# Performance work log

Measured on AMD Instinct MI355X. Metric: run time of the kernel, lower is better.

Reference implementation:

```python
import jax, jax.numpy as jnp
import numpy as np

S, D_MODEL, D_K = 4096, 1024, 64
SCALE = float(np.sqrt(D_K))


def setup_inputs() -> dict:
    key = jax.random.key(0)
    ks = jax.random.split(key, 7)
    def p(k, shape, fan_in):
        # torch nn.Linear default init: U(-1/sqrt(fan_in), 1/sqrt(fan_in))
        lim = 1.0 / np.sqrt(fan_in)
        return jax.random.uniform(k, shape, jnp.float32, -lim, lim)
    return {
        "x": jax.random.normal(ks[0], (S, D_MODEL), jnp.float32),
        "Wq": p(ks[1], (D_K, D_MODEL), D_MODEL),
        "bq": p(ks[2], (D_K,), D_MODEL),
        "Wk": p(ks[3], (D_K, D_MODEL), D_MODEL),
        "bk": p(ks[4], (D_K,), D_MODEL),
        "Wv": p(ks[5], (D_K, D_MODEL), D_MODEL),
        "bv": p(ks[6], (D_K,), D_MODEL),
    }


def reference(x, Wq, bq, Wk, bk, Wv, bv):
    # Linear projections: y = x @ W.T + b  (torch nn.Linear convention)
    Q = x @ Wq.T + bq          # [S, d_k]
    K = x @ Wk.T + bk          # [S, d_k]
    V = x @ Wv.T + bv          # [S, d_k]
    scores = (Q @ K.T) / SCALE  # [S, S]
    # causal mask: -inf strictly above the diagonal (triu(1))
    row = jnp.arange(S)[:, None]
    col = jnp.arange(S)[None, :]
    scores = jnp.where(col > row, -jnp.inf, scores)
    attn = jax.nn.softmax(scores, axis=1)
    return attn @ V            # [S, d_k]
```

## Files before the change

### kernel.cpp

```cpp
#include <hip/hip_runtime.h>

#define SS 4096
#define DM 1024

typedef __attribute__((ext_vector_type(4))) float f32x4;
typedef __attribute__((ext_vector_type(8))) __bf16 bf16x8;
typedef __attribute__((ext_vector_type(8))) unsigned short ushort8;
typedef __attribute__((ext_vector_type(4))) unsigned short ushort4v;

#define NEGHUGE -3.0e38f
#define LOG2E 1.44269504f

__device__ __forceinline__ unsigned short f2b(float f) {
    unsigned u = __builtin_bit_cast(unsigned, f);
    u += 0x7fffu + ((u >> 16) & 1u);
    return (unsigned short)(u >> 16);
}

__device__ __forceinline__ f32x4 mfma16(ushort8 a, ushort8 b, f32x4 c) {
    return __builtin_amdgcn_mfma_f32_16x16x32_bf16(
        __builtin_bit_cast(bf16x8, a), __builtin_bit_cast(bf16x8, b), c, 0, 0, 0);
}

__global__ __launch_bounds__(256) void convw_kernel(
    const float* __restrict__ Wq, const float* __restrict__ Wk,
    const float* __restrict__ Wv, unsigned short* __restrict__ wb)
{
    int i = (blockIdx.x * 256 + threadIdx.x) * 4;
    const float* src;
    if (i < 65536) src = Wq + i;
    else if (i < 131072) src = Wk + (i - 65536);
    else src = Wv + (i - 131072);
    f32x4 v = *reinterpret_cast<const f32x4*>(src);
    ushort4v o;
    o[0] = f2b(v[0]); o[1] = f2b(v[1]); o[2] = f2b(v[2]); o[3] = f2b(v[3]);
    *reinterpret_cast<ushort4v*>(wb + i) = o;
}

__global__ __launch_bounds__(512) void proj_kernel(
    const float* __restrict__ x, const unsigned short* __restrict__ wb,
    const float* __restrict__ bq, const float* __restrict__ bk, const float* __restrict__ bv,
    unsigned short* __restrict__ Qs, unsigned short* __restrict__ Kb,
    unsigned short* __restrict__ VT)
{
    __shared__ float comb[8 * 3072];
    const int m0 = blockIdx.x * 16;
    const int tid = threadIdx.x;
    const int w = tid >> 6, l = tid & 63;
    const int lc = l & 15;
    const int lk = (l >> 4) * 8;

    f32x4 acc[12] = {};
    const float* xrow = x + (m0 + lc) * DM;
    const int kbase = w * 128;

    for (int kk = 0; kk < 128; kk += 32) {
        const int k0 = kbase + kk + lk;
        f32x4 u = *reinterpret_cast<const f32x4*>(xrow + k0);
        f32x4 v = *reinterpret_cast<const f32x4*>(xrow + k0 + 4);
        ushort8 a;
        a[0] = f2b(u[0]); a[1] = f2b(u[1]); a[2] = f2b(u[2]); a[3] = f2b(u[3]);
        a[4] = f2b(v[0]); a[5] = f2b(v[1]); a[6] = f2b(v[2]); a[7] = f2b(v[3]);
#pragma unroll
        for (int nf = 0; nf < 12; nf++) {
            ushort8 b = *reinterpret_cast<const ushort8*>(wb + (nf * 16 + lc) * DM + k0);
            acc[nf] = mfma16(a, b, acc[nf]);
        }
    }

#pragma unroll
    for (int nf = 0; nf < 12; nf++)
#pragma unroll
        for (int r = 0; r < 4; r++) {
            int row = (l >> 4) * 4 + r;
            comb[w * 3072 + row * 192 + nf * 16 + lc] = acc[nf][r];
        }
    __syncthreads();

    for (int idx = tid; idx < 3072; idx += 512) {
        int row = idx / 192, col = idx % 192;
        float s = 0.f;
#pragma unroll
        for (int ww = 0; ww < 8; ww++) s += comb[ww * 3072 + idx];
        int grow = m0 + row;
        if (col < 64) {
            s += bq[col];
            Qs[grow * 64 + col] = f2b(s * 0.125f);
        } else if (col < 128) {
            s += bk[col - 64];
            Kb[grow * 64 + col - 64] = f2b(s);
        } else {
            s += bv[col - 128];
            VT[(col - 128) * SS + grow] = f2b(s);
        }
    }
}

__global__ __launch_bounds__(256) void attn_part_kernel(
    const unsigned short* __restrict__ Qs, const unsigned short* __restrict__ Kb,
    const unsigned short* __restrict__ VT, float* __restrict__ part)
{
    __shared__ unsigned short plds[4][16 * 64];
    __shared__ float comb[4][16 * 66];

    const int bid = blockIdx.x;
    const int g = bid >> 2, c = bid & 3;
    const int q0 = g * 16;
    const int tid = threadIdx.x;
    const int w = tid >> 6, l = tid & 63;
    const int lc = l & 15;
    const int lg4 = l >> 4;
    const int lk = lg4 * 8;

    const int T = g / 4 + 1;
    const int W0 = c * 4 + w;

    ushort8 aq0 = *reinterpret_cast<const ushort8*>(Qs + (q0 + lc) * 64 + lk);
    ushort8 aq1 = *reinterpret_cast<const ushort8*>(Qs + (q0 + lc) * 64 + 32 + lk);

    float m4[4], l4[4];
    f32x4 o[4] = {};
#pragma unroll
    for (int r = 0; r < 4; r++) { m4[r] = NEGHUGE; l4[r] = 0.f; }

    char* myp = reinterpret_cast<char*>(plds[w]);

    for (int t = W0; t < T; t += 16) {
        const int kv0 = t * 64;
        f32x4 s[4] = {};
#pragma unroll
        for (int nf = 0; nf < 4; nf++) {
            const unsigned short* kr = Kb + (kv0 + nf * 16 + lc) * 64;
            ushort8 b0 = *reinterpret_cast<const ushort8*>(kr + lk);
            ushort8 b1 = *reinterpret_cast<const ushort8*>(kr + 32 + lk);
            s[nf] = mfma16(aq0, b0, s[nf]);
            s[nf] = mfma16(aq1, b1, s[nf]);
        }
        if (kv0 + 63 > q0) {
#pragma unroll
            for (int nf = 0; nf < 4; nf++)
#pragma unroll
                for (int r = 0; r < 4; r++) {
                    int colg = kv0 + nf * 16 + lc;
                    int rowg = q0 + lg4 * 4 + r;
                    if (colg > rowg) s[nf][r] = NEGHUGE;
                }
        }
#pragma unroll
        for (int r = 0; r < 4; r++) {
            float mx = fmaxf(fmaxf(s[0][r], s[1][r]), fmaxf(s[2][r], s[3][r]));
            mx = fmaxf(mx, __shfl_xor(mx, 1));
            mx = fmaxf(mx, __shfl_xor(mx, 2));
            mx = fmaxf(mx, __shfl_xor(mx, 4));
            mx = fmaxf(mx, __shfl_xor(mx, 8));
            float mn = fmaxf(m4[r], mx);
            float sc = exp2f((m4[r] - mn) * LOG2E);
            m4[r] = mn;
            float rs = 0.f;
#pragma unroll
            for (int nf = 0; nf < 4; nf++) {
                float p = exp2f((s[nf][r] - mn) * LOG2E);
                s[nf][r] = p;
                rs += p;
            }
            rs += __shfl_xor(rs, 1);
            rs += __shfl_xor(rs, 2);
            rs += __shfl_xor(rs, 4);
            rs += __shfl_xor(rs, 8);
            l4[r] = l4[r] * sc + rs;
            o[0][r] *= sc; o[1][r] *= sc; o[2][r] *= sc; o[3][r] *= sc;
        }
#pragma unroll
        for (int nf = 0; nf < 4; nf++)
#pragma unroll
            for (int r = 0; r < 4; r++) {
                int row = lg4 * 4 + r;
                int byte = (row * 128 + (nf * 16 + lc) * 2) ^ ((row & 7) << 4);
                *reinterpret_cast<unsigned short*>(myp + byte) = f2b(s[nf][r]);
            }
        asm volatile("s_waitcnt lgkmcnt(0)" ::: "memory");
        __builtin_amdgcn_sched_barrier(0);
#pragma unroll
        for (int k = 0; k < 2; k++) {
            int rbyte = (lc * 128 + (k * 32 + lk) * 2) ^ ((lc & 7) << 4);
            ushort8 pa = *reinterpret_cast<const ushort8*>(myp + rbyte);
#pragma unroll
            for (int df = 0; df < 4; df++) {
                ushort8 bv = *reinterpret_cast<const ushort8*>(
                    VT + (df * 16 + lc) * SS + kv0 + k * 32 + lk);
                o[df] = mfma16(pa, bv, o[df]);
            }
        }
    }

#pragma unroll
    for (int df = 0; df < 4; df++)
#pragma unroll
        for (int r = 0; r < 4; r++)
            comb[w][(lg4 * 4 + r) * 66 + df * 16 + lc] = o[df][r];
    if (lc == 0) {
#pragma unroll
        for (int r = 0; r < 4; r++) {
            comb[w][(lg4 * 4 + r) * 66 + 64] = m4[r];
            comb[w][(lg4 * 4 + r) * 66 + 65] = l4[r];
        }
    }
    __syncthreads();

    float* pp = part + bid * 1056;
    for (int idx = tid; idx < 1024; idx += 256) {
        int row = idx >> 6, col = idx & 63;
        float M = fmaxf(fmaxf(comb[0][row * 66 + 64], comb[1][row * 66 + 64]),
                        fmaxf(comb[2][row * 66 + 64], comb[3][row * 66 + 64]));
        float val = 0.f, den = 0.f;
#pragma unroll
        for (int ww = 0; ww < 4; ww++) {
            float f = exp2f((comb[ww][row * 66 + 64] - M) * LOG2E);
            val += comb[ww][row * 66 + col] * f;
            den += comb[ww][row * 66 + 65] * f;
        }
        pp[row * 66 + col] = val;
        if (col == 0) {
            pp[row * 66 + 64] = M;
            pp[row * 66 + 65] = den;
        }
    }
}

__global__ __launch_bounds__(256) void attn_comb_kernel(
    const float* __restrict__ part, float* __restrict__ out)
{
    const int g = blockIdx.x;
    const int q0 = g * 16;
    const float* p0 = part + (g * 4) * 1056;
    for (int idx = threadIdx.x; idx < 1024; idx += 256) {
        int row = idx >> 6, col = idx & 63;
        float M = NEGHUGE;
#pragma unroll
        for (int cc = 0; cc < 4; cc++)
            M = fmaxf(M, p0[cc * 1056 + row * 66 + 64]);
        float val = 0.f, den = 0.f;
#pragma unroll
        for (int cc = 0; cc < 4; cc++) {
            float f = exp2f((p0[cc * 1056 + row * 66 + 64] - M) * LOG2E);
            val += p0[cc * 1056 + row * 66 + col] * f;
            den += p0[cc * 1056 + row * 66 + 65] * f;
        }
        out[(q0 + row) * 64 + col] = val / den;
    }
}

extern "C" void kernel_launch(void* const* d_in, const int* in_sizes, int n_in,
                              void* d_out, int out_size, void* d_ws, size_t ws_size,
                              hipStream_t stream) {
    const float* x  = (const float*)d_in[0];
    const float* Wq = (const float*)d_in[1];
    const float* bq = (const float*)d_in[2];
    const float* Wk = (const float*)d_in[3];
    const float* bk = (const float*)d_in[4];
    const float* Wv = (const float*)d_in[5];
    const float* bv = (const float*)d_in[6];
    float* out = (float*)d_out;

    char* ws = (char*)d_ws;
    unsigned short* wb = (unsigned short*)ws;
    unsigned short* Qs = (unsigned short*)(ws + 393216);
    unsigned short* Kb = (unsigned short*)(ws + 917504);
    unsigned short* VT = (unsigned short*)(ws + 1441792);
    float* part = (float*)(ws + 1966080);

    convw_kernel<<<dim3(192), dim3(256), 0, stream>>>(Wq, Wk, Wv, wb);
    proj_kernel<<<dim3(256), dim3(512), 0, stream>>>(x, wb, bq, bk, bv, Qs, Kb, VT);
    attn_part_kernel<<<dim3(1024), dim3(256), 0, stream>>>(Qs, Kb, VT, part);
    attn_comb_kernel<<<dim3(256), dim3(256), 0, stream>>>(part, out);
}
```

Baseline: 56.03 us.

## Process 32 query rows per attention block, split KV eight ways, reverse block order

The attention partial kernel now handles 32 query rows per block as two 16-row MFMA tiles that share each K and V fragment load, which halves K/V global traffic per query row. The KV range is split across 8 blocks of 4 waves, and blocks are ordered so the heaviest causal rows launch first. The combine kernel is adjusted to match. The projection kernel is also cut to 4 waves, each doing twice the K-depth, with a padded LDS reduction buffer. The trade-offs are higher register pressure from doubled accumulators and more partial results to merge.

```diff
diff --git a/kernel.cpp b/kernel.cpp
--- a/kernel.cpp
+++ b/kernel.cpp
@@ -2,6 +2,9 @@
 
 #define SS 4096
 #define DM 1024
+#define QBLK 32
+#define CH 8
+#define PSTRIDE 2112
 
 typedef __attribute__((ext_vector_type(4))) float f32x4;
 typedef __attribute__((ext_vector_type(8))) __bf16 bf16x8;
@@ -37,13 +40,13 @@
     *reinterpret_cast<ushort4v*>(wb + i) = o;
 }
 
-__global__ __launch_bounds__(512) void proj_kernel(
+__global__ __launch_bounds__(256) void proj_kernel(
     const float* __restrict__ x, const unsigned short* __restrict__ wb,
     const float* __restrict__ bq, const float* __restrict__ bk, const float* __restrict__ bv,
     unsigned short* __restrict__ Qs, unsigned short* __restrict__ Kb,
     unsigned short* __restrict__ VT)
 {
-    __shared__ float comb[8 * 3072];
+    __shared__ float comb[4 * 16 * 196];
     const int m0 = blockIdx.x * 16;
     const int tid = threadIdx.x;
     const int w = tid >> 6, l = tid & 63;
@@ -52,9 +55,9 @@
 
     f32x4 acc[12] = {};
     const float* xrow = x + (m0 + lc) * DM;
-    const int kbase = w * 128;
-
-    for (int kk = 0; kk < 128; kk += 32) {
+    const int kbase = w * 256;
+
+    for (int kk = 0; kk < 256; kk += 32) {
         const int k0 = kbase + kk + lk;
         f32x4 u = *reinterpret_cast<const f32x4*>(xrow + k0);
         f32x4 v = *reinterpret_cast<const f32x4*>(xrow + k0 + 4);
@@ -73,15 +76,14 @@
 #pragma unroll
         for (int r = 0; r < 4; r++) {
             int row = (l >> 4) * 4 + r;
-            comb[w * 3072 + row * 192 + nf * 16 + lc] = acc[nf][r];
+            comb[w * 3136 + row * 196 + nf * 16 + lc] = acc[nf][r];
         }
     __syncthreads();
 
-    for (int idx = tid; idx < 3072; idx += 512) {
+    for (int idx = tid; idx < 3072; idx += 256) {
         int row = idx / 192, col = idx % 192;
-        float s = 0.f;
-#pragma unroll
-        for (int ww = 0; ww < 8; ww++) s += comb[ww * 3072 + idx];
+        int off = row * 196 + col;
+        float s = comb[off] + comb[3136 + off] + comb[6272 + off] + comb[9408 + off];
         int grow = m0 + row;
         if (col < 64) {
             s += bq[col];
@@ -100,115 +102,141 @@
     const unsigned short* __restrict__ Qs, const unsigned short* __restrict__ Kb,
     const unsigned short* __restrict__ VT, float* __restrict__ part)
 {
-    __shared__ unsigned short plds[4][16 * 64];
-    __shared__ float comb[4][16 * 66];
+    __shared__ unsigned short plds[4][QBLK * 64];
+    __shared__ float comb[4][QBLK * 66];
 
     const int bid = blockIdx.x;
-    const int g = bid >> 2, c = bid & 3;
-    const int q0 = g * 16;
+    const int g = 127 - (bid >> 3);
+    const int c = bid & 7;
+    const int q0 = g * QBLK;
     const int tid = threadIdx.x;
     const int w = tid >> 6, l = tid & 63;
     const int lc = l & 15;
     const int lg4 = l >> 4;
     const int lk = lg4 * 8;
 
-    const int T = g / 4 + 1;
+    const int T = (g + 2) >> 1;
     const int W0 = c * 4 + w;
 
-    ushort8 aq0 = *reinterpret_cast<const ushort8*>(Qs + (q0 + lc) * 64 + lk);
-    ushort8 aq1 = *reinterpret_cast<const ushort8*>(Qs + (q0 + lc) * 64 + 32 + lk);
-
-    float m4[4], l4[4];
-    f32x4 o[4] = {};
-#pragma unroll
-    for (int r = 0; r < 4; r++) { m4[r] = NEGHUGE; l4[r] = 0.f; }
+    ushort8 aq[2][2];
+#pragma unroll
+    for (int rs = 0; rs < 2; rs++) {
+        aq[rs][0] = *reinterpret_cast<const ushort8*>(Qs + (q0 + rs * 16 + lc) * 64 + lk);
+        aq[rs][1] = *reinterpret_cast<const ushort8*>(Qs + (q0 + rs * 16 + lc) * 64 + 32 + lk);
+    }
+
+    float m4[2][4], l4[2][4];
+    f32x4 o[2][4] = {};
+#pragma unroll
+    for (int rs = 0; rs < 2; rs++)
+#pragma unroll
+        for (int r = 0; r < 4; r++) { m4[rs][r] = NEGHUGE; l4[rs][r] = 0.f; }
 
     char* myp = reinterpret_cast<char*>(plds[w]);
 
-    for (int t = W0; t < T; t += 16) {
+    for (int t = W0; t < T; t += 32) {
         const int kv0 = t * 64;
-        f32x4 s[4] = {};
+        f32x4 s[2][4] = {};
 #pragma unroll
         for (int nf = 0; nf < 4; nf++) {
             const unsigned short* kr = Kb + (kv0 + nf * 16 + lc) * 64;
             ushort8 b0 = *reinterpret_cast<const ushort8*>(kr + lk);
             ushort8 b1 = *reinterpret_cast<const ushort8*>(kr + 32 + lk);
-            s[nf] = mfma16(aq0, b0, s[nf]);
-            s[nf] = mfma16(aq1, b1, s[nf]);
+            s[0][nf] = mfma16(aq[0][0], b0, s[0][nf]);
+            s[0][nf] = mfma16(aq[0][1], b1, s[0][nf]);
+            s[1][nf] = mfma16(aq[1][0], b0, s[1][nf]);
+            s[1][nf] = mfma16(aq[1][1], b1, s[1][nf]);
         }
         if (kv0 + 63 > q0) {
 #pragma unroll
+            for (int rs = 0; rs < 2; rs++)
+#pragma unroll
+                for (int nf = 0; nf < 4; nf++)
+#pragma unroll
+                    for (int r = 0; r < 4; r++) {
+                        int colg = kv0 + nf * 16 + lc;
+                        int rowg = q0 + rs * 16 + lg4 * 4 + r;
+                        if (colg > rowg) s[rs][nf][r] = NEGHUGE;
+                    }
+        }
+#pragma unroll
+        for (int rs = 0; rs < 2; rs++)
+#pragma unroll
+            for (int r = 0; r < 4; r++) {
+                float mx = fmaxf(fmaxf(s[rs][0][r], s[rs][1][r]),
+                                 fmaxf(s[rs][2][r], s[rs][3][r]));
+                mx = fmaxf(mx, __shfl_xor(mx, 1));
+                mx = fmaxf(mx, __shfl_xor(mx, 2));
+                mx = fmaxf(mx, __shfl_xor(mx, 4));
+                mx = fmaxf(mx, __shfl_xor(mx, 8));
+                float mn = fmaxf(m4[rs][r], mx);
+                float sc = exp2f((m4[rs][r] - mn) * LOG2E);
+                m4[rs][r] = mn;
+                float rsum = 0.f;
+#pragma unroll
+                for (int nf = 0; nf < 4; nf++) {
+                    float p = exp2f((s[rs][nf][r] - mn) * LOG2E);
+                    s[rs][nf][r] = p;
+                    rsum += p;
+                }
+                rsum += __shfl_xor(rsum, 1);
+                rsum += __shfl_xor(rsum, 2);
+                rsum += __shfl_xor(rsum, 4);
+                rsum += __shfl_xor(rsum, 8);
+                l4[rs][r] = l4[rs][r] * sc + rsum;
+                o[rs][0][r] *= sc; o[rs][1][r] *= sc;
+                o[rs][2][r] *= sc; o[rs][3][r] *= sc;
+            }
+#pragma unroll
+        for (int rs = 0; rs < 2; rs++)
+#pragma unroll
             for (int nf = 0; nf < 4; nf++)
 #pragma unroll
                 for (int r = 0; r < 4; r++) {
-                    int colg = kv0 + nf * 16 + lc;
-                    int rowg = q0 + lg4 * 4 + r;
-                    if (colg > rowg) s[nf][r] = NEGHUGE;
+                    int row = rs * 16 + lg4 * 4 + r;
+                    int byte = (row * 128 + (nf * 16 + lc) * 2) ^ ((row & 7) << 4);
+                    *reinterpret_cast<unsigned short*>(myp + byte) = f2b(s[rs][nf][r]);
                 }
-        }
-#pragma unroll
-        for (int r = 0; r < 4; r++) {
-            float mx = fmaxf(fmaxf(s[0][r], s[1][r]), fmaxf(s[2][r], s[3][r]));
-            mx = fmaxf(mx, __shfl_xor(mx, 1));
-            mx = fmaxf(mx, __shfl_xor(mx, 2));
-            mx = fmaxf(mx, __shfl_xor(mx, 4));
-            mx = fmaxf(mx, __shfl_xor(mx, 8));
-            float mn = fmaxf(m4[r], mx);
-            float sc = exp2f((m4[r] - mn) * LOG2E);
-            m4[r] = mn;
-            float rs = 0.f;
-#pragma unroll
-            for (int nf = 0; nf < 4; nf++) {
-                float p = exp2f((s[nf][r] - mn) * LOG2E);
-                s[nf][r] = p;
-                rs += p;
-            }
-            rs += __shfl_xor(rs, 1);
-            rs += __shfl_xor(rs, 2);
-            rs += __shfl_xor(rs, 4);
-            rs += __shfl_xor(rs, 8);
-            l4[r] = l4[r] * sc + rs;
-            o[0][r] *= sc; o[1][r] *= sc; o[2][r] *= sc; o[3][r] *= sc;
-        }
-#pragma unroll
-        for (int nf = 0; nf < 4; nf++)
-#pragma unroll
-            for (int r = 0; r < 4; r++) {
-                int row = lg4 * 4 + r;
-                int byte = (row * 128 + (nf * 16 + lc) * 2) ^ ((row & 7) << 4);
-                *reinterpret_cast<unsigned short*>(myp + byte) = f2b(s[nf][r]);
-            }
         asm volatile("s_waitcnt lgkmcnt(0)" ::: "memory");
         __builtin_amdgcn_sched_barrier(0);
 #pragma unroll
         for (int k = 0; k < 2; k++) {
-            int rbyte = (lc * 128 + (k * 32 + lk) * 2) ^ ((lc & 7) << 4);
-            ushort8 pa = *reinterpret_cast<const ushort8*>(myp + rbyte);
+            ushort8 pa0, pa1;
+            {
+                int rb0 = ((lc) * 128 + (k * 32 + lk) * 2) ^ ((lc & 7) << 4);
+                int rb1 = ((16 + lc) * 128 + (k * 32 + lk) * 2) ^ ((lc & 7) << 4);
+                pa0 = *reinterpret_cast<const ushort8*>(myp + rb0);
+                pa1 = *reinterpret_cast<const ushort8*>(myp + rb1);
+            }
 #pragma unroll
             for (int df = 0; df < 4; df++) {
                 ushort8 bv = *reinterpret_cast<const ushort8*>(
                     VT + (df * 16 + lc) * SS + kv0 + k * 32 + lk);
-                o[df] = mfma16(pa, bv, o[df]);
+                o[0][df] = mfma16(pa0, bv, o[0][df]);
+                o[1][df] = mfma16(pa1, bv, o[1][df]);
             }
         }
     }
 
 #pragma unroll
-    for (int df = 0; df < 4; df++)
-#pragma unroll
-        for (int r = 0; r < 4; r++)
-            comb[w][(lg4 * 4 + r) * 66 + df * 16 + lc] = o[df][r];
-    if (lc == 0) {
-#pragma unroll
-        for (int r = 0; r < 4; r++) {
-            comb[w][(lg4 * 4 + r) * 66 + 64] = m4[r];
-            comb[w][(lg4 * 4 + r) * 66 + 65] = l4[r];
+    for (int rs = 0; rs < 2; rs++) {
+#pragma unroll
+        for (int df = 0; df < 4; df++)
+#pragma unroll
+            for (int r = 0; r < 4; r++)
+                comb[w][(rs * 16 + lg4 * 4 + r) * 66 + df * 16 + lc] = o[rs][df][r];
+        if (lc == 0) {
+#pragma unroll
+            for (int r = 0; r < 4; r++) {
+                comb[w][(rs * 16 + lg4 * 4 + r) * 66 + 64] = m4[rs][r];
+                comb[w][(rs * 16 + lg4 * 4 + r) * 66 + 65] = l4[rs][r];
+            }
         }
     }
     __syncthreads();
 
-    float* pp = part + bid * 1056;
-    for (int idx = tid; idx < 1024; idx += 256) {
+    float* pp = part + bid * PSTRIDE;
+    for (int idx = tid; idx < QBLK * 64; idx += 256) {
         int row = idx >> 6, col = idx & 63;
         float M = fmaxf(fmaxf(comb[0][row * 66 + 64], comb[1][row * 66 + 64]),
                         fmaxf(comb[2][row * 66 + 64], comb[3][row * 66 + 64]));
@@ -230,21 +258,22 @@
 __global__ __launch_bounds__(256) void attn_comb_kernel(
     const float* __restrict__ part, float* __restrict__ out)
 {
-    const int g = blockIdx.x;
-    const int q0 = g * 16;
-    const float* p0 = part + (g * 4) * 1056;
-    for (int idx = threadIdx.x; idx < 1024; idx += 256) {
+    const int b = blockIdx.x;
+    const int g = 127 - b;
+    const int q0 = g * QBLK;
+    const float* p0 = part + (b * CH) * PSTRIDE;
+    for (int idx = threadIdx.x; idx < QBLK * 64; idx += 256) {
         int row = idx >> 6, col = idx & 63;
         float M = NEGHUGE;
 #pragma unroll
-        for (int cc = 0; cc < 4; cc++)
-            M = fmaxf(M, p0[cc * 1056 + row * 66 + 64]);
+        for (int cc = 0; cc < CH; cc++)
+            M = fmaxf(M, p0[cc * PSTRIDE + row * 66 + 64]);
         float val = 0.f, den = 0.f;
 #pragma unroll
-        for (int cc = 0; cc < 4; cc++) {
-            float f = exp2f((p0[cc * 1056 + row * 66 + 64] - M) * LOG2E);
-            val += p0[cc * 1056 + row * 66 + col] * f;
-            den += p0[cc * 1056 + row * 66 + 65] * f;
+        for (int cc = 0; cc < CH; cc++) {
+            float f = exp2f((p0[cc * PSTRIDE + row * 66 + 64] - M) * LOG2E);
+            val += p0[cc * PSTRIDE + row * 66 + col] * f;
+            den += p0[cc * PSTRIDE + row * 66 + 65] * f;
         }
         out[(q0 + row) * 64 + col] = val / den;
     }
@@ -270,7 +299,7 @@
     float* part = (float*)(ws + 1966080);
 
     convw_kernel<<<dim3(192), dim3(256), 0, stream>>>(Wq, Wk, Wv, wb);
-    proj_kernel<<<dim3(256), dim3(512), 0, stream>>>(x, wb, bq, bk, bv, Qs, Kb, VT);
+    proj_kernel<<<dim3(256), dim3(256), 0, stream>>>(x, wb, bq, bk, bv, Qs, Kb, VT);
     attn_part_kernel<<<dim3(1024), dim3(256), 0, stream>>>(Qs, Kb, VT, part);
-    attn_comb_kernel<<<dim3(256), dim3(256), 0, stream>>>(part, out);
-}
+    attn_comb_kernel<<<dim3(128), dim3(256), 0, stream>>>(part, out);
+}
```

After: 64.94 us. +15.9%, slower.
